# Kernel tuning notes

Measured on AMD Instinct MI355X. Metric: run time of the kernel, lower is better.

Reference implementation:

```python
import jax, jax.numpy as jnp
import numpy as np

H, C = 4, 32            # heads, per-head out channels -> H*C = 128
NEG = jnp.float32(-1e9) # stand-in for -inf mask (keeps grads finite)
NUM_LOC = 15            # self.num_locations hardcoded to 15


def _tconv(x, src, dst, ea, Wq, bq, Wk, bk, Wv, bv, We, Ws, bs, Wb):
    # PyG TransformerConv(beta=True, concat=True, edge_dim=1)
    N = x.shape[0]
    q = (x @ Wq + bq).reshape(N, H, C)
    k = (x @ Wk + bk).reshape(N, H, C)
    v = (x @ Wv + bv).reshape(N, H, C)
    e = (ea @ We).reshape(-1, H, C)  # edge embedding [E,H,C]
    kj = k[src] + e
    alpha = jnp.einsum('ehc,ehc->eh', q[dst], kj) / jnp.sqrt(jnp.float32(C))
    # scatter-softmax over incoming edges of each dst node
    amax = jax.ops.segment_max(alpha, dst, num_segments=N)
    ex = jnp.exp(alpha - amax[dst])
    den = jax.ops.segment_sum(ex, dst, num_segments=N)
    w = ex / (den[dst] + 1e-16)
    out = jax.ops.segment_sum((v[src] + e) * w[..., None], dst, num_segments=N).reshape(N, H * C)
    xr = x @ Ws + bs  # lin_skip
    beta = jax.nn.sigmoid(jnp.concatenate([out, xr, out - xr], axis=-1) @ Wb)  # [N,1]
    return beta * xr + (1.0 - beta) * out


def _bn(x, g, b):
    # BatchNorm1d in training mode (batch statistics, biased var)
    m = x.mean(0)
    v = ((x - m) ** 2).mean(0)
    return (x - m) * jax.lax.rsqrt(v + 1e-5) * g + b


def _forward_core(fa, edge_index, active_mask):
    (node_type, requests, latency,
     c0_Wq, c0_bq, c0_Wk, c0_bk, c0_Wv, c0_bv, c0_We, c0_Ws, c0_bs, c0_Wb,
     t0_W, t0_b, bn0_g, bn0_b,
     cs_Wq, cs_bq, cs_Wk, cs_bk, cs_Wv, cs_bv, cs_We, cs_Ws, cs_bs, cs_Wb,
     ts_W, ts_b, bns_g, bns_b,
     emb_W1, emb_b1, emb_W2, emb_b2, emb_W3, emb_b3,
     rem_W, rem_b, add_W, add_b) = fa
    src, dst = edge_index[0], edge_index[1]
    ea = latency[:, None]                      # edge_attr [E,1]
    x = jnp.stack([node_type, requests], axis=1)  # [N,2]
    # NetworkGraphEmbeddingConstructor: conv1 + 4 stacked conv/linear/bn blocks
    x = _tconv(x, src, dst, ea, c0_Wq, c0_bq, c0_Wk, c0_bk, c0_Wv, c0_bv, c0_We, c0_Ws, c0_bs, c0_Wb)
    x = _bn(jax.nn.relu(x @ t0_W + t0_b), bn0_g, bn0_b)
    for i in range(4):
        x = _tconv(x, src, dst, ea, cs_Wq[i], cs_bq[i], cs_Wk[i], cs_bk[i], cs_Wv[i], cs_bv[i], cs_We[i], cs_Ws[i], cs_bs[i], cs_Wb[i])
        x = _bn(jax.nn.relu(x @ ts_W[i] + ts_b[i]), bns_g[i], bns_b[i])
    # embedding_transformation MLP
    x = jax.nn.relu(x @ emb_W1 + emb_b1)
    x = jax.nn.relu(x @ emb_W2 + emb_b2)
    x = x @ emb_W3 + emb_b3                    # [N,64]
    # sampling head (batch_index=None branch)
    N = x.shape[0]
    maskf = jnp.where(active_mask == 1, jnp.float32(0.0), NEG)
    loc = jnp.arange(N) < NUM_LOC
    remove_mask = jnp.where(loc, jnp.where(maskf == 0.0, NEG, jnp.float32(0.0)), maskf)
    logits1 = (x @ rem_W + rem_b)[:, 0] + remove_mask
    k1, k2 = jax.random.split(jax.random.key(42))
    a1 = jnp.argmax(logits1 + jax.random.gumbel(k1, (N,), logits1.dtype))  # Categorical sample
    mask2 = maskf.at[a1].set(0.0)
    t = jnp.tanh(x[a1] @ add_W + add_b)        # [64]
    logits2 = x @ t + mask2
    a2 = jnp.argmax(logits2 + jax.random.gumbel(k2, (N,), logits2.dtype))
    log_probs = jnp.stack([jax.nn.log_softmax(logits1)[a1], jax.nn.log_softmax(logits2)[a2]])
    return jnp.stack([logits1, logits2]), jnp.stack([a1, a2]), log_probs


def setup_inputs() -> dict:
    N, E = 50000, 400000
    F, HC, EMB, L = 2, 128, 32, 4
    key = jax.random.key(0)
    kit = iter(jax.random.split(key, 64))
    def w(shape, s=0.1):
        return jax.random.normal(next(kit), shape, jnp.float32) * s
    return {
        'node_type': w((N,), 1.0),
        'requests': jax.random.uniform(next(kit), (N,), jnp.float32),
        'latency': jax.random.uniform(next(kit), (E,), jnp.float32),
        'edge_index': jax.random.randint(next(kit), (2, E), 0, N, jnp.int32),
        'active_mask': jax.random.randint(next(kit), (N,), 0, 2, jnp.int32),
        'c0_Wq': w((F, HC)), 'c0_bq': w((HC,)),
        'c0_Wk': w((F, HC)), 'c0_bk': w((HC,)),
        'c0_Wv': w((F, HC)), 'c0_bv': w((HC,)),
        'c0_We': w((1, HC)),
        'c0_Ws': w((F, HC)), 'c0_bs': w((HC,)),
        'c0_Wb': w((3 * HC, 1)),
        't0_W': w((HC, EMB)), 't0_b': w((EMB,)),
        'bn0_g': jnp.ones((EMB,), jnp.float32), 'bn0_b': jnp.zeros((EMB,), jnp.float32),
        'cs_Wq': w((L, EMB, HC)), 'cs_bq': w((L, HC)),
        'cs_Wk': w((L, EMB, HC)), 'cs_bk': w((L, HC)),
        'cs_Wv': w((L, EMB, HC)), 'cs_bv': w((L, HC)),
        'cs_We': w((L, 1, HC)),
        'cs_Ws': w((L, EMB, HC)), 'cs_bs': w((L, HC)),
        'cs_Wb': w((L, 3 * HC, 1)),
        'ts_W': w((L, HC, EMB)), 'ts_b': w((L, EMB)),
        'bns_g': jnp.ones((L, EMB), jnp.float32), 'bns_b': jnp.zeros((L, EMB), jnp.float32),
        'emb_W1': w((EMB, 128)), 'emb_b1': w((128,)),
        'emb_W2': w((128, 64)), 'emb_b2': w((64,)),
        'emb_W3': w((64, 64)), 'emb_b3': w((64,)),
        'rem_W': w((64, 1)), 'rem_b': w((1,)),
        'add_W': w((64, 64)), 'add_b': w((64,)),
    }


def reference(node_type, requests, latency, edge_index, active_mask,
              c0_Wq, c0_bq, c0_Wk, c0_bk, c0_Wv, c0_bv, c0_We, c0_Ws, c0_bs, c0_Wb,
              t0_W, t0_b, bn0_g, bn0_b,
              cs_Wq, cs_bq, cs_Wk, cs_bk, cs_Wv, cs_bv, cs_We, cs_Ws, cs_bs, cs_Wb,
              ts_W, ts_b, bns_g, bns_b,
              emb_W1, emb_b1, emb_W2, emb_b2, emb_W3, emb_b3,
              rem_W, rem_b, add_W, add_b):
    fa = (node_type, requests, latency,
          c0_Wq, c0_bq, c0_Wk, c0_bk, c0_Wv, c0_bv, c0_We, c0_Ws, c0_bs, c0_Wb,
          t0_W, t0_b, bn0_g, bn0_b,
          cs_Wq, cs_bq, cs_Wk, cs_bk, cs_Wv, cs_bv, cs_We, cs_Ws, cs_bs, cs_Wb,
          ts_W, ts_b, bns_g, bns_b,
          emb_W1, emb_b1, emb_W2, emb_b2, emb_W3, emb_b3,
          rem_W, rem_b, add_W, add_b)
    return _forward_core(fa, edge_index, active_mask)
```

## Files before the change

kernel.cpp:

```cpp
#include <hip/hip_runtime.h>
#include <hip/hip_fp16.h>
#include <cstdint>
#include <math.h>

typedef _Float16 h2 __attribute__((ext_vector_type(2)));
typedef float f32x2 __attribute__((ext_vector_type(2)));

__device__ __forceinline__ h2 f2h2(float a, float b) {
    h2 r; r.x = (_Float16)a; r.y = (_Float16)b; return r;
}
__device__ __forceinline__ float fdot2f(h2 a, h2 b, float c) {
    return __builtin_amdgcn_fdot2(a, b, c, false);
}
__device__ __forceinline__ f32x2 bc2(float x) { f32x2 r; r.x = x; r.y = x; return r; }
__device__ __forceinline__ f32x2 cvt2(h2 v) {
    f32x2 r; r.x = (float)v.x; r.y = (float)v.y; return r;
}
__device__ __forceinline__ f32x2 mk2(float a, float b) { f32x2 r; r.x = a; r.y = b; return r; }

union f4h {
    float4 f;
    h2 h[4];
    __half2 u[4];
};

__device__ __forceinline__ uint32_t rotl32(uint32_t x, uint32_t n) {
    return (x << n) | (x >> (32u - n));
}

__device__ __forceinline__ void tf2x32(uint32_t k0, uint32_t k1,
                                       uint32_t x0, uint32_t x1,
                                       uint32_t& o0, uint32_t& o1) {
    uint32_t k2 = k0 ^ k1 ^ 0x1BD11BDAu;
    x0 += k0; x1 += k1;
    x0 += x1; x1 = rotl32(x1, 13); x1 ^= x0;
    x0 += x1; x1 = rotl32(x1, 15); x1 ^= x0;
    x0 += x1; x1 = rotl32(x1, 26); x1 ^= x0;
    x0 += x1; x1 = rotl32(x1, 6);  x1 ^= x0;
    x0 += k1; x1 += k2 + 1u;
    x0 += x1; x1 = rotl32(x1, 17); x1 ^= x0;
    x0 += x1; x1 = rotl32(x1, 29); x1 ^= x0;
    x0 += x1; x1 = rotl32(x1, 16); x1 ^= x0;
    x0 += x1; x1 = rotl32(x1, 24); x1 ^= x0;
    x0 += k2; x1 += k0 + 2u;
    x0 += x1; x1 = rotl32(x1, 13); x1 ^= x0;
    x0 += x1; x1 = rotl32(x1, 15); x1 ^= x0;
    x0 += x1; x1 = rotl32(x1, 26); x1 ^= x0;
    x0 += x1; x1 = rotl32(x1, 6);  x1 ^= x0;
    x0 += k0; x1 += k1 + 3u;
    x0 += x1; x1 = rotl32(x1, 17); x1 ^= x0;
    x0 += x1; x1 = rotl32(x1, 29); x1 ^= x0;
    x0 += x1; x1 = rotl32(x1, 16); x1 ^= x0;
    x0 += x1; x1 = rotl32(x1, 24); x1 ^= x0;
    x0 += k1; x1 += k2 + 4u;
    x0 += x1; x1 = rotl32(x1, 13); x1 ^= x0;
    x0 += x1; x1 = rotl32(x1, 15); x1 ^= x0;
    x0 += x1; x1 = rotl32(x1, 26); x1 ^= x0;
    x0 += x1; x1 = rotl32(x1, 6);  x1 ^= x0;
    x0 += k2; x1 += k0 + 5u;
    o0 = x0; o1 = x1;
}

__device__ float gumbel_at(int n, int which, int N) {
    uint32_t a0, a1, b0, b1;
    tf2x32(0u, 42u, 0u, 2u, a0, a1);
    tf2x32(0u, 42u, 1u, 3u, b0, b1);
    uint32_t gk0 = which ? a1 : a0;
    uint32_t gk1 = which ? b1 : b0;
    int half = N >> 1;
    uint32_t o0, o1, bits;
    if (n < half) { tf2x32(gk0, gk1, (uint32_t)n, (uint32_t)(n + half), o0, o1); bits = o0; }
    else          { tf2x32(gk0, gk1, (uint32_t)(n - half), (uint32_t)n, o0, o1); bits = o1; }
    float f = __uint_as_float((bits >> 9) | 0x3F800000u) - 1.0f;
    float u = fmaxf(1.17549435e-38f, f);
    return -logf(-logf(u));
}

__device__ __forceinline__ uint32_t fmono(float f) {
    uint32_t b = __float_as_uint(f);
    return (b & 0x80000000u) ? ~b : (b | 0x80000000u);
}
__device__ __forceinline__ float funmono(uint32_t u) {
    uint32_t b = (u & 0x80000000u) ? (u & 0x7FFFFFFFu) : ~u;
    return __uint_as_float(b);
}

#define NEGF (-1e9f)
#define ATTNGRID 2048

__global__ void k_hist(const int* __restrict__ dstp, int* __restrict__ deg, int E) {
    int e = blockIdx.x * 256 + threadIdx.x;
    if (e < E) atomicAdd(&deg[dstp[e]], 1);
}

__global__ void k_scan1(const int* __restrict__ deg, int* __restrict__ bsum, int N) {
    __shared__ int s[256];
    int i = blockIdx.x * 256 + threadIdx.x;
    s[threadIdx.x] = (i < N) ? deg[i] : 0;
    __syncthreads();
    for (int st = 128; st > 0; st >>= 1) {
        if (threadIdx.x < st) s[threadIdx.x] += s[threadIdx.x + st];
        __syncthreads();
    }
    if (threadIdx.x == 0) bsum[blockIdx.x] = s[0];
}

__global__ void k_scan2(int* __restrict__ bsum, int nb) {
    __shared__ int s[256];
    int i = threadIdx.x;
    int v = (i < nb) ? bsum[i] : 0;
    s[i] = v;
    __syncthreads();
    for (int st = 1; st < 256; st <<= 1) {
        int t = (i >= st) ? s[i - st] : 0;
        __syncthreads();
        s[i] += t;
        __syncthreads();
    }
    if (i < nb) bsum[i] = s[i] - v;
}

__global__ void k_scan3(const int* __restrict__ deg, const int* __restrict__ bsum,
                        int* __restrict__ rowptr, int* __restrict__ cursor, int N) {
    __shared__ int s[256];
    int i = blockIdx.x * 256 + threadIdx.x;
    int v = (i < N) ? deg[i] : 0;
    s[threadIdx.x] = v;
    __syncthreads();
    for (int st = 1; st < 256; st <<= 1) {
        int t = (threadIdx.x >= st) ? s[threadIdx.x - st] : 0;
        __syncthreads();
        s[threadIdx.x] += t;
        __syncthreads();
    }
    int excl = s[threadIdx.x] - v + bsum[blockIdx.x];
    if (i < N) { rowptr[i] = excl; cursor[i] = excl; }
}

__global__ void k_fill(const int* __restrict__ dstp, const int* __restrict__ srcp,
                       const float* __restrict__ lat, int* __restrict__ cursor,
                       int2* __restrict__ srclat, int E) {
    int e = blockIdx.x * 256 + threadIdx.x;
    if (e < E) {
        int pos = atomicAdd(&cursor[dstp[e]], 1);
        srclat[pos] = make_int2(srcp[e], __float_as_int(lat[e]));
    }
}

__global__ __launch_bounds__(512, 4) void k_qkvr(
        const float* __restrict__ xin, const float* __restrict__ nt,
        const float* __restrict__ rq, int din, int N,
        const float* __restrict__ Wq, const float* __restrict__ bq,
        const float* __restrict__ Wk, const float* __restrict__ bk,
        const float* __restrict__ Wv, const float* __restrict__ bv,
        const float* __restrict__ Ws, const float* __restrict__ bs,
        const double* __restrict__ SUM, const double* __restrict__ SUMSQ,
        const float* __restrict__ bng, const float* __restrict__ bnb,
        int applyBN,
        __half* __restrict__ Q, __half* __restrict__ KV, __half* __restrict__ R) {
    __shared__ h2 w2[4][16 * 128];
    __shared__ float bias[4][128];
    __shared__ h2 xs2[32][17];
    __shared__ float sscale[32], sshift[32];
    int t = threadIdx.x;
    int dpCount = din >> 1;
    for (int i = t; i < dpCount * 128; i += 512) {
        int dp = i >> 7, j = i & 127;
        w2[0][i] = f2h2(Wq[(size_t)(2 * dp) * 128 + j], Wq[(size_t)(2 * dp + 1) * 128 + j]);
        w2[1][i] = f2h2(Wk[(size_t)(2 * dp) * 128 + j], Wk[(size_t)(2 * dp + 1) * 128 + j]);
        w2[2][i] = f2h2(Wv[(size_t)(2 * dp) * 128 + j], Wv[(size_t)(2 * dp + 1) * 128 + j]);
        w2[3][i] = f2h2(Ws[(size_t)(2 * dp) * 128 + j], Ws[(size_t)(2 * dp + 1) * 128 + j]);
    }
    if (t < 128) {
        bias[0][t] = bq[t]; bias[1][t] = bk[t]; bias[2][t] = bv[t]; bias[3][t] = bs[t];
    }
    if (t < 32) {
        if (applyBN) {
            double m = SUM[t] / N;
            double v = SUMSQ[t] / N - m * m;
            float inv = rsqrtf((float)v + 1e-5f);
            float sc = inv * bng[t];
            sscale[t] = sc;
            sshift[t] = bnb[t] - (float)m * sc;
        } else {
            sscale[t] = 1.f; sshift[t] = 0.f;
        }
    }
    int quad = t & 31;
    int sub = t >> 5;
    int dpsh = (din == 32) ? 4 : 0;
    int tiles = (N + 31) >> 5;
    for (int tile = blockIdx.x; tile < tiles; tile += gridDim.x) {
        int base = tile << 5;
        __syncthreads();
        for (int i = t; i < 32 * dpCount; i += 512) {
            int nl = i >> dpsh, dp = i & (dpCount - 1);
            int nn = base + nl;
            float x0 = 0.f, x1 = 0.f;
            if (nn < N) {
                if (din == 2) { x0 = nt[nn]; x1 = rq[nn]; }
                else {
                    x0 = xin[(size_t)nn * din + 2 * dp];
                    x1 = xin[(size_t)nn * din + 2 * dp + 1];
                }
            }
            x0 = x0 * sscale[2 * dp] + sshift[2 * dp];
            x1 = x1 * sscale[2 * dp + 1] + sshift[2 * dp + 1];
            xs2[nl][dp] = f2h2(x0, x1);
        }
        __syncthreads();
        float acc[4][2][4];
#pragma unroll
        for (int m = 0; m < 4; ++m)
#pragma unroll
            for (int k = 0; k < 2; ++k)
#pragma unroll
                for (int c = 0; c < 4; ++c) acc[m][k][c] = bias[m][quad * 4 + c];
        for (int dp = 0; dp < dpCount; ++dp) {
            h2 xv0 = xs2[sub * 2 + 0][dp];
            h2 xv1 = xs2[sub * 2 + 1][dp];
#pragma unroll
            for (int m = 0; m < 4; ++m) {
                const h2* wp = &w2[m][dp * 128 + quad * 4];
                h2 wa = wp[0], wb = wp[1], wc = wp[2], wd = wp[3];
                acc[m][0][0] = fdot2f(xv0, wa, acc[m][0][0]);
                acc[m][0][1] = fdot2f(xv0, wb, acc[m][0][1]);
                acc[m][0][2] = fdot2f(xv0, wc, acc[m][0][2]);
                acc[m][0][3] = fdot2f(xv0, wd, acc[m][0][3]);
                acc[m][1][0] = fdot2f(xv1, wa, acc[m][1][0]);
                acc[m][1][1] = fdot2f(xv1, wb, acc[m][1][1]);
                acc[m][1][2] = fdot2f(xv1, wc, acc[m][1][2]);
                acc[m][1][3] = fdot2f(xv1, wd, acc[m][1][3]);
            }
        }
#pragma unroll
        for (int k = 0; k < 2; ++k) {
            int n = base + sub * 2 + k;
            if (n < N) {
                *(__half2*)&Q[(size_t)n * 128 + quad * 4 + 0] =
// ... 164 lines not shown
        float inv = 1.f / (den + 1e-16f);
        f32x2 inv2 = bc2(inv), pls2 = bc2(plsum);
        f32x2 O0 = (A0 + pls2 * wep[0]) * inv2;
        f32x2 O1 = (A1 + pls2 * wep[1]) * inv2;
        f32x2 O2 = (A2 + pls2 * wep[2]) * inv2;
        f32x2 O3 = (A3 + pls2 * wep[3]) * inv2;

        f32x2 R0 = cvt2(rh.h[0]), R1 = cvt2(rh.h[1]);
        f32x2 R2 = cvt2(rh.h[2]), R3 = cvt2(rh.h[3]);
        f32x2 G = O0 * bop[0];
        G += R0 * brp[0];
        G += O1 * bop[1]; G += R1 * brp[1];
        G += O2 * bop[2]; G += R2 * brp[2];
        G += O3 * bop[3]; G += R3 * brp[3];
        float g = G.x + G.y;
        g += __shfl_xor(g, 1); g += __shfl_xor(g, 2);
        g += __shfl_xor(g, 4); g += __shfl_xor(g, 8);
        float beta = 1.0f / (1.0f + __expf(-g));

        if ((l64 & 16) == 0 && n < N) {
            f32x2 bb = bc2(beta), ib = bc2(1.0f - beta);
            f32x2 W0 = bb * R0 + ib * O0;
            f32x2 W1 = bb * R1 + ib * O1;
            f32x2 W2 = bb * R2 + ib * O2;
            f32x2 W3 = bb * R3 + ib * O3;
            *(__half2*)&A[(size_t)n * 128 + lane * 8 + 0] = __floats2half2_rn(W0.x, W0.y);
            *(__half2*)&A[(size_t)n * 128 + lane * 8 + 2] = __floats2half2_rn(W1.x, W1.y);
            *(__half2*)&A[(size_t)n * 128 + lane * 8 + 4] = __floats2half2_rn(W2.x, W2.y);
            *(__half2*)&A[(size_t)n * 128 + lane * 8 + 6] = __floats2half2_rn(W3.x, W3.y);
        }

        qh.f = pq.f; rh.f = pr.f; k0.f = pk.f; v0.f = pv.f; l0 = pl;
        start = s1; d = d1;
        s1 = s2; d1 = d2; s2 = s3; d2 = d3;
        psl1 = psl2;
    }
}

__global__ __launch_bounds__(256) void k_linstats(
        const __half* __restrict__ A, const float* __restrict__ tW,
        const float* __restrict__ tb, float* __restrict__ H32,
        double* __restrict__ partials, int N) {
    __shared__ h2 w2l[64 * 32];
    __shared__ float bias[32];
    __shared__ h2 xsT[64][66];
    __shared__ double sp1[4][8][4], sp2[4][8][4];
    int t = threadIdx.x;
    for (int i = t; i < 64 * 32; i += 256) {
        int dp = i >> 5, j = i & 31;
        w2l[i] = f2h2(tW[(size_t)(2 * dp) * 32 + j], tW[(size_t)(2 * dp + 1) * 32 + j]);
    }
    if (t < 32) bias[t] = tb[t];
    int quad = t & 7;
    int sub = t >> 3;
    int base = blockIdx.x << 6;

    __syncthreads();
#pragma unroll
    for (int k = 0; k < 4; ++k) {
        int i = t + 256 * k;
        int nl = i >> 4, g8 = i & 15;
        int n = base + nl;
        h2 hv[4];
        if (n < N) {
            const h2* ap = (const h2*)(A + (size_t)n * 128 + g8 * 8);
            hv[0] = ap[0]; hv[1] = ap[1]; hv[2] = ap[2]; hv[3] = ap[3];
        } else {
            h2 z; z.x = (_Float16)0.f; z.y = (_Float16)0.f;
            hv[0] = z; hv[1] = z; hv[2] = z; hv[3] = z;
        }
        xsT[g8 * 4 + 0][nl] = hv[0];
        xsT[g8 * 4 + 1][nl] = hv[1];
        xsT[g8 * 4 + 2][nl] = hv[2];
        xsT[g8 * 4 + 3][nl] = hv[3];
    }
    __syncthreads();

    float acc[2][4];
#pragma unroll
    for (int k = 0; k < 2; ++k)
#pragma unroll
        for (int c = 0; c < 4; ++c) acc[k][c] = bias[quad * 4 + c];
    for (int dp = 0; dp < 64; ++dp) {
        h2 x0 = xsT[dp][sub * 2 + 0];
        h2 x1 = xsT[dp][sub * 2 + 1];
        const h2* wp = &w2l[dp * 32 + quad * 4];
        h2 wa = wp[0], wb = wp[1], wc = wp[2], wd = wp[3];
        acc[0][0] = fdot2f(x0, wa, acc[0][0]);
        acc[0][1] = fdot2f(x0, wb, acc[0][1]);
        acc[0][2] = fdot2f(x0, wc, acc[0][2]);
        acc[0][3] = fdot2f(x0, wd, acc[0][3]);
        acc[1][0] = fdot2f(x1, wa, acc[1][0]);
        acc[1][1] = fdot2f(x1, wb, acc[1][1]);
        acc[1][2] = fdot2f(x1, wc, acc[1][2]);
        acc[1][3] = fdot2f(x1, wd, acc[1][3]);
    }
    double s1[4] = {0, 0, 0, 0}, s2[4] = {0, 0, 0, 0};
#pragma unroll
    for (int k = 0; k < 2; ++k) {
        int n = base + sub * 2 + k;
        if (n < N) {
            float4 yv;
            yv.x = fmaxf(acc[k][0], 0.f); yv.y = fmaxf(acc[k][1], 0.f);
            yv.z = fmaxf(acc[k][2], 0.f); yv.w = fmaxf(acc[k][3], 0.f);
            *(float4*)&H32[(size_t)n * 32 + quad * 4] = yv;
            s1[0] += yv.x; s1[1] += yv.y; s1[2] += yv.z; s1[3] += yv.w;
            s2[0] += (double)yv.x * yv.x; s2[1] += (double)yv.y * yv.y;
            s2[2] += (double)yv.z * yv.z; s2[3] += (double)yv.w * yv.w;
        }
    }
#pragma unroll
    for (int c = 0; c < 4; ++c) {
        s1[c] += __shfl_xor(s1[c], 8);  s2[c] += __shfl_xor(s2[c], 8);
        s1[c] += __shfl_xor(s1[c], 16); s2[c] += __shfl_xor(s2[c], 16);
        s1[c] += __shfl_xor(s1[c], 32); s2[c] += __shfl_xor(s2[c], 32);
    }
    __syncthreads();
    int wave = t >> 6;
    if ((t & 63) < 8) {
#pragma unroll
        for (int c = 0; c < 4; ++c) { sp1[wave][quad][c] = s1[c]; sp2[wave][quad][c] = s2[c]; }
    }
    __syncthreads();
    if (t < 32) {
        int q = t >> 2, c = t & 3;
        double a1 = 0, a2 = 0;
#pragma unroll
        for (int wv = 0; wv < 4; ++wv) { a1 += sp1[wv][q][c]; a2 += sp2[wv][q][c]; }
        partials[(size_t)blockIdx.x * 64 + t] = a1;
        partials[(size_t)blockIdx.x * 64 + 32 + t] = a2;
    }
}

__global__ void k_statred(const double* __restrict__ partials,
                          double* __restrict__ SUM, double* __restrict__ SUMSQ,
                          int nblocks) {
    __shared__ double s[256];
    int col = blockIdx.x;
    double a = 0;
    for (int b = threadIdx.x; b < nblocks; b += 256)
        a += partials[(size_t)b * 64 + col];
    s[threadIdx.x] = a;
    __syncthreads();
    for (int st = 128; st > 0; st >>= 1) {
        if (threadIdx.x < st) s[threadIdx.x] += s[threadIdx.x + st];
        __syncthreads();
    }
    if (threadIdx.x == 0) {
        if (col < 32) SUM[col] = s[0];
        else SUMSQ[col - 32] = s[0];
    }
}

__global__ __launch_bounds__(256) void k_mlp1(
        const float* __restrict__ H32,
        const double* __restrict__ SUM, const double* __restrict__ SUMSQ,
        const float* __restrict__ bng, const float* __restrict__ bnb,
        const float* __restrict__ W1, const float* __restrict__ b1,
        float* __restrict__ Y1, unsigned int* __restrict__ smallbuf, int N) {
    __shared__ float w1[32 * 128];
    __shared__ float sb1[128];
    __shared__ float sscale[32], sshift[32];
    __shared__ float xs[32][36];
    int t = threadIdx.x;
    if (blockIdx.x == 0 && t < 16) smallbuf[t] = 0u;
    for (int i = t; i < 32 * 128; i += 256) w1[i] = W1[i];
    if (t < 128) sb1[t] = b1[t];
    if (t < 32) {
        double m = SUM[t] / N;
        double v = SUMSQ[t] / N - m * m;
        float inv = rsqrtf((float)v + 1e-5f);
        float sc = inv * bng[t];
        sscale[t] = sc;
        sshift[t] = bnb[t] - (float)m * sc;
    }
    int quad = t & 31, sub = t >> 5;
    int tiles = (N + 31) >> 5;
    for (int tile = blockIdx.x; tile < tiles; tile += gridDim.x) {
        int base = tile << 5;
        __syncthreads();
        {
            int nl = t >> 3, q = t & 7;
            int n = base + nl;
            float4 xv = make_float4(0.f, 0.f, 0.f, 0.f);
            if (n < N) xv = *(const float4*)&H32[(size_t)n * 32 + q * 4];
            xs[nl][q * 4 + 0] = xv.x * sscale[q * 4 + 0] + sshift[q * 4 + 0];
            xs[nl][q * 4 + 1] = xv.y * sscale[q * 4 + 1] + sshift[q * 4 + 1];
            xs[nl][q * 4 + 2] = xv.z * sscale[q * 4 + 2] + sshift[q * 4 + 2];
            xs[nl][q * 4 + 3] = xv.w * sscale[q * 4 + 3] + sshift[q * 4 + 3];
        }
        __syncthreads();
        float a[4][4];
#pragma unroll
        for (int k = 0; k < 4; ++k)
#pragma unroll
            for (int c = 0; c < 4; ++c) a[k][c] = sb1[quad * 4 + c];
        for (int d = 0; d < 32; ++d) {
            float4 w4 = *(const float4*)&w1[d * 128 + quad * 4];
#pragma unroll
            for (int k = 0; k < 4; ++k) {
                float x = xs[sub * 4 + k][d];
                a[k][0] = fmaf(x, w4.x, a[k][0]);
                a[k][1] = fmaf(x, w4.y, a[k][1]);
                a[k][2] = fmaf(x, w4.z, a[k][2]);
                a[k][3] = fmaf(x, w4.w, a[k][3]);
            }
        }
#pragma unroll
        for (int k = 0; k < 4; ++k) {
            int n = base + sub * 4 + k;
            if (n < N) {
                float4 yv;
                yv.x = fmaxf(a[k][0], 0.f); yv.y = fmaxf(a[k][1], 0.f);
                yv.z = fmaxf(a[k][2], 0.f); yv.w = fmaxf(a[k][3], 0.f);
                *(float4*)&Y1[(size_t)n * 128 + quad * 4] = yv;
            }
        }
    }
}

__global__ __launch_bounds__(256) void k_mlp2(
        const float* __restrict__ Y1, const float* __restrict__ W2,
        const float* __restrict__ b2, float* __restrict__ Y2, int N) {
    __shared__ float w2f[128 * 64];
    __shared__ float sb2[64];
    __shared__ float xs[32][132];
    int t = threadIdx.x;
    for (int i = t; i < 128 * 64; i += 256) w2f[i] = W2[i];
    if (t < 64) sb2[t] = b2[t];
    int quad = t & 15, sub = t >> 4;
    int tiles = (N + 31) >> 5;
    for (int tile = blockIdx.x; tile < tiles; tile += gridDim.x) {
        int base = tile << 5;
        __syncthreads();
#pragma unroll
        for (int k = 0; k < 4; ++k) {
            int i = t + 256 * k;
            int nl = i >> 5, q = i & 31;
            int n = base + nl;
            float4 xv = make_float4(0.f, 0.f, 0.f, 0.f);
            if (n < N) xv = *(const float4*)&Y1[(size_t)n * 128 + q * 4];
            *(float4*)&xs[nl][q * 4] = xv;
        }
        __syncthreads();
        float a[2][4];
#pragma unroll
        for (int k = 0; k < 2; ++k)
#pragma unroll
            for (int c = 0; c < 4; ++c) a[k][c] = sb2[quad * 4 + c];
        for (int d = 0; d < 128; ++d) {
            float4 w4 = *(const float4*)&w2f[d * 64 + quad * 4];
#pragma unroll
            for (int k = 0; k < 2; ++k) {
                float x = xs[sub * 2 + k][d];
                a[k][0] = fmaf(x, w4.x, a[k][0]);
                a[k][1] = fmaf(x, w4.y, a[k][1]);
                a[k][2] = fmaf(x, w4.z, a[k][2]);
                a[k][3] = fmaf(x, w4.w, a[k][3]);
            }
        }
#pragma unroll
        for (int k = 0; k < 2; ++k) {
            int n = base + sub * 2 + k;
            if (n < N) {
                float4 yv;
                yv.x = fmaxf(a[k][0], 0.f); yv.y = fmaxf(a[k][1], 0.f);
                yv.z = fmaxf(a[k][2], 0.f); yv.w = fmaxf(a[k][3], 0.f);
                *(float4*)&Y2[(size_t)n * 64 + quad * 4] = yv;
            }
        }
    }
}

__global__ __launch_bounds__(256) void k_mlp3(
        const float* __restrict__ Y2, const float* __restrict__ W3,
        const float* __restrict__ b3, float* __restrict__ X3, int N) {
    __shared__ float w3[64 * 64];
    __shared__ float sb3[64];
    __shared__ float xs[32][68];
    int t = threadIdx.x;
    for (int i = t; i < 64 * 64; i += 256) w3[i] = W3[i];
    if (t < 64) sb3[t] = b3[t];
    int quad = t & 15, sub = t >> 4;
    int tiles = (N + 31) >> 5;
    for (int tile = blockIdx.x; tile < tiles; tile += gridDim.x) {
        int base = tile << 5;
        __syncthreads();
#pragma unroll
        for (int k = 0; k < 2; ++k) {
            int i = t + 256 * k;
            int nl = i >> 4, q = i & 15;
            int n = base + nl;
            float4 xv = make_float4(0.f, 0.f, 0.f, 0.f);
            if (n < N) xv = *(const float4*)&Y2[(size_t)n * 64 + q * 4];
            *(float4*)&xs[nl][q * 4] = xv;
        }
        __syncthreads();
        float a[2][4];
#pragma unroll
        for (int k = 0; k < 2; ++k)
#pragma unroll
            for (int c = 0; c < 4; ++c) a[k][c] = sb3[quad * 4 + c];
        for (int d = 0; d < 64; ++d) {
            float4 w4 = *(const float4*)&w3[d * 64 + quad * 4];
#pragma unroll
            for (int k = 0; k < 2; ++k) {
                float x = xs[sub * 2 + k][d];
                a[k][0] = fmaf(x, w4.x, a[k][0]);
                a[k][1] = fmaf(x, w4.y, a[k][1]);
                a[k][2] = fmaf(x, w4.z, a[k][2]);
                a[k][3] = fmaf(x, w4.w, a[k][3]);
            }
        }
#pragma unroll
        for (int k = 0; k < 2; ++k) {
            int n = base + sub * 2 + k;
            if (n < N)
                *(float4*)&X3[(size_t)n * 64 + quad * 4] = *(float4*)a[k];
        }
    }
}

__global__ void k_head1(const float* __restrict__ X3, const float* __restrict__ remW,
                        const float* __restrict__ remB, const int* __restrict__ active,
                        float* __restrict__ l1out, unsigned long long* __restrict__ slot1,
                        unsigned int* __restrict__ m1, int N) {
    int n = blockIdx.x * 256 + threadIdx.x;
    if (n >= N) return;
    const float* xr = X3 + (size_t)n * 64;
    float acc = remB[0];
    for (int d = 0; d < 64; d++) acc = fmaf(xr[d], remW[d], acc);
    float maskf = (active[n] == 1) ? 0.f : NEGF;
    float rm = (n < 15) ? ((maskf == 0.f) ? NEGF : 0.f) : maskf;
    float l1 = acc + rm;
    l1out[n] = l1;
    atomicMax(m1, fmono(l1));
    float z = l1 + gumbel_at(n, 0, N);
    unsigned long long p = ((unsigned long long)fmono(z) << 32) |
                           (unsigned long long)(0xFFFFFFFFu - (unsigned)n);
    atomicMax(slot1, p);
}

__global__ void k_head2(const float* __restrict__ X3, const float* __restrict__ addW,
                        const float* __restrict__ addB,
                        const unsigned long long* __restrict__ slot1,
                        float* __restrict__ tvec, int* __restrict__ a1buf) {
    int j = threadIdx.x;
    unsigned long long p = *slot1;
    int a1 = (int)(0xFFFFFFFFu - (unsigned)(p & 0xFFFFFFFFull));
    const float* xr = X3 + (size_t)a1 * 64;
    float acc = addB[j];
    for (int d = 0; d < 64; d++) acc = fmaf(xr[d], addW[d * 64 + j], acc);
    tvec[j] = tanhf(acc);
    if (j == 0) *a1buf = a1;
}

__global__ void k_head3(const float* __restrict__ X3, const float* __restrict__ tvec,
                        const int* __restrict__ active, const int* __restrict__ a1buf,
                        float* __restrict__ l2out, unsigned long long* __restrict__ slot2,
                        unsigned int* __restrict__ m2, int N) {
    int n = blockIdx.x * 256 + threadIdx.x;
    if (n >= N) return;
    const float* xr = X3 + (size_t)n * 64;
    float acc = 0.f;
    for (int d = 0; d < 64; d++) acc = fmaf(xr[d], tvec[d], acc);
    float maskf = (active[n] == 1) ? 0.f : NEGF;
    if (n == *a1buf) maskf = 0.f;
    float l2 = acc + maskf;
    l2out[n] = l2;
    atomicMax(m2, fmono(l2));
    float z = l2 + gumbel_at(n, 1, N);
    unsigned long long p = ((unsigned long long)fmono(z) << 32) |
                           (unsigned long long)(0xFFFFFFFFu - (unsigned)n);
    atomicMax(slot2, p);
}

__global__ void k_sumexp(const float* __restrict__ l1, const float* __restrict__ l2,
                         const unsigned int* __restrict__ m1, const unsigned int* __restrict__ m2,
                         float* __restrict__ se, int N) {
    int t = blockIdx.x * 256 + threadIdx.x;
    float M1 = funmono(*m1), M2 = funmono(*m2);
    float e1 = 0.f, e2 = 0.f;
    if (t < N) { e1 = expf(l1[t] - M1); e2 = expf(l2[t] - M2); }
    __shared__ float r1[256], r2[256];
    r1[threadIdx.x] = e1; r2[threadIdx.x] = e2;
    __syncthreads();
    for (int s = 128; s > 0; s >>= 1) {
        if (threadIdx.x < s) { r1[threadIdx.x] += r1[threadIdx.x + s]; r2[threadIdx.x] += r2[threadIdx.x + s]; }
        __syncthreads();
    }
    if (threadIdx.x == 0) { atomicAdd(&se[0], r1[0]); atomicAdd(&se[1], r2[0]); }
}

__global__ void k_final(const float* __restrict__ l1, const float* __restrict__ l2,
                        const unsigned long long* __restrict__ slot2,
                        const int* __restrict__ a1buf,
                        const unsigned int* __restrict__ m1, const unsigned int* __restrict__ m2,
                        const float* __restrict__ se, float* __restrict__ outTail, int N) {
    int a1 = *a1buf;
    int a2 = (int)(0xFFFFFFFFu - (unsigned)((*slot2) & 0xFFFFFFFFull));
    outTail[0] = (float)a1;
    outTail[1] = (float)a2;
    outTail[2] = l1[a1] - (funmono(*m1) + logf(se[0]));
    outTail[3] = l2[a2] - (funmono(*m2) + logf(se[1]));
}

extern "C" void kernel_launch(void* const* d_in, const int* in_sizes, int n_in,
                              void* d_out, int out_size, void* d_ws, size_t ws_size,
                              hipStream_t stream) {
    const float* node_type = (const float*)d_in[0];
    const float* requests  = (const float*)d_in[1];
    const float* latency   = (const float*)d_in[2];
    const int* edge_index  = (const int*)d_in[3];
    const int* active      = (const int*)d_in[4];
    int N = in_sizes[0];
    int E = in_sizes[2];
    const int* src = edge_index;
    const int* dst = edge_index + E;
    float* out = (float*)d_out;

    char* base = (char*)d_ws;
    size_t off = 0;
    auto alloc = [&](size_t bytes) -> char* {
        char* p = base + off;
        off += (bytes + 255) & ~(size_t)255;
        return p;
    };
    char* Abuf   = alloc((size_t)N * 128 * 4);
    char* Qbuf   = alloc((size_t)N * 128 * 4);
    __half* KV   = (__half*)alloc((size_t)N * 256 * 2);
    char* Rbuf   = alloc((size_t)N * 128 * 4);
    float* H32   = (float*)alloc((size_t)N * 32 * 4);
    int* deg     = (int*)alloc((size_t)N * 4);
    int* rowptr  = (int*)alloc((size_t)N * 4);
    int* cursor  = (int*)alloc((size_t)N * 4);
    int2* srclat = (int2*)alloc((size_t)E * 8);
    int* bsum    = (int*)alloc(1024 * 4);
    int lsTiles = (N + 63) / 64;
    double* partials = (double*)alloc((size_t)lsTiles * 64 * 8);
    double* SUM  = (double*)alloc(512);
    double* SUMSQ = SUM + 32;
    char* small  = alloc(1024);
    unsigned long long* slot1 = (unsigned long long*)small;
    unsigned long long* slot2 = slot1 + 1;
    unsigned int* m1 = (unsigned int*)(small + 16);
    unsigned int* m2 = m1 + 1;
    float* se = (float*)(small + 24);
    int* a1buf = (int*)(small + 32);
    float* tvec = (float*)(small + 64);

    __half* Ah = (__half*)Abuf;   float* Y2f = (float*)Abuf;
    __half* Qh = (__half*)Qbuf;   float* Y1f = (float*)Qbuf;
    __half* Rh = (__half*)Rbuf;   float* X3f = (float*)Rbuf;

    int ng = (N + 255) / 256;
    int egE = (E + 255) / 256;
    int nb = ng;

    (void)hipMemsetAsync(deg, 0, (size_t)N * 4, stream);
    k_hist<<<egE, 256, 0, stream>>>(dst, deg, E);
    k_scan1<<<nb, 256, 0, stream>>>(deg, bsum, N);
    k_scan2<<<1, 256, 0, stream>>>(bsum, nb);
    k_scan3<<<nb, 256, 0, stream>>>(deg, bsum, rowptr, cursor, N);
    k_fill<<<egE, 256, 0, stream>>>(dst, src, latency, cursor, srclat, E);

    for (int L = 0; L < 5; ++L) {
        int din = L ? 32 : 2;
        const float* xin = L ? H32 : nullptr;
        const float* Wq = L ? (const float*)d_in[19] + (size_t)(L - 1) * 4096 : (const float*)d_in[5];
        const float* bq = L ? (const float*)d_in[20] + (size_t)(L - 1) * 128  : (const float*)d_in[6];
        const float* Wk = L ? (const float*)d_in[21] + (size_t)(L - 1) * 4096 : (const float*)d_in[7];
        const float* bk = L ? (const float*)d_in[22] + (size_t)(L - 1) * 128  : (const float*)d_in[8];
        const float* Wv = L ? (const float*)d_in[23] + (size_t)(L - 1) * 4096 : (const float*)d_in[9];
        const float* bv = L ? (const float*)d_in[24] + (size_t)(L - 1) * 128  : (const float*)d_in[10];
        const float* We = L ? (const float*)d_in[25] + (size_t)(L - 1) * 128  : (const float*)d_in[11];
        const float* Ws = L ? (const float*)d_in[26] + (size_t)(L - 1) * 4096 : (const float*)d_in[12];
        const float* bs = L ? (const float*)d_in[27] + (size_t)(L - 1) * 128  : (const float*)d_in[13];
        const float* Wb = L ? (const float*)d_in[28] + (size_t)(L - 1) * 384  : (const float*)d_in[14];
        const float* tW = L ? (const float*)d_in[29] + (size_t)(L - 1) * 4096 : (const float*)d_in[15];
        const float* tb = L ? (const float*)d_in[30] + (size_t)(L - 1) * 32   : (const float*)d_in[16];
        const float* bngP = (L == 1) ? (const float*)d_in[17]
                          : (L >= 2) ? (const float*)d_in[31] + (size_t)(L - 2) * 32 : nullptr;
        const float* bnbP = (L == 1) ? (const float*)d_in[18]
                          : (L >= 2) ? (const float*)d_in[32] + (size_t)(L - 2) * 32 : nullptr;

        k_qkvr<<<1024, 512, 0, stream>>>(xin, node_type, requests, din, N,
                                         Wq, bq, Wk, bk, Wv, bv, Ws, bs,
                                         SUM, SUMSQ, bngP, bnbP, (L > 0) ? 1 : 0,
                                         Qh, KV, Rh);
        k_attn<<<ATTNGRID, 256, 0, stream>>>(srclat, Qh, KV, We, Rh, Wb,
                                             rowptr, deg, Ah, N);
        k_linstats<<<lsTiles, 256, 0, stream>>>(Ah, tW, tb, H32, partials, N);
        k_statred<<<64, 256, 0, stream>>>(partials, SUM, SUMSQ, lsTiles);
    }

    k_mlp1<<<512, 256, 0, stream>>>(H32, SUM, SUMSQ,
                                    (const float*)d_in[31] + 3 * 32,
                                    (const float*)d_in[32] + 3 * 32,
                                    (const float*)d_in[33], (const float*)d_in[34],
                                    Y1f, (unsigned int*)small, N);
    k_mlp2<<<512, 256, 0, stream>>>(Y1f, (const float*)d_in[35], (const float*)d_in[36],
                                    Y2f, N);
    k_mlp3<<<512, 256, 0, stream>>>(Y2f, (const float*)d_in[37], (const float*)d_in[38],
                                    X3f, N);
    k_head1<<<ng, 256, 0, stream>>>(X3f, (const float*)d_in[39], (const float*)d_in[40],
                                    active, out, slot1, m1, N);
    k_head2<<<1, 64, 0, stream>>>(X3f, (const float*)d_in[41], (const float*)d_in[42],
                                  slot1, tvec, a1buf);
    k_head3<<<ng, 256, 0, stream>>>(X3f, tvec, active, a1buf, out + N, slot2, m2, N);
    k_sumexp<<<ng, 256, 0, stream>>>(out, out + N, m1, m2, se, N);
    k_final<<<1, 1, 0, stream>>>(out, out + N, slot2, a1buf, m1, m2, se, out + 2 * N, N);
}
```

Measured before the change: 713.5 us.

## Fuse MLP layers and head kernels with online log-sum-exp partial reductions

Fuses MLP layers 1 and 2 into one kernel that keeps the 128-wide hidden activations in shared memory, and folds the removal-head logit computation into the layer-3 kernel. The global-atomic max plus separate sum-exp pass is replaced by per-block online log-sum-exp partials merged in a final block-wide kernel. This removes the Y1 global round trip, several launches and contended atomics, but the fused kernel uses more shared memory, which may lower occupancy, and it now processes 16-node tiles.

```diff
diff --git a/kernel.cpp b/kernel.cpp
--- a/kernel.cpp
+++ b/kernel.cpp
@@ -85,6 +85,13 @@
     return __uint_as_float(b);
 }
 
+__device__ __forceinline__ void lse_merge(float& m, float& s, float m2, float s2) {
+    float M = fmaxf(m, m2);
+    float a = (m == -INFINITY) ? 0.f : expf(m - M) * s;
+    float b = (m2 == -INFINITY) ? 0.f : expf(m2 - M) * s2;
+    m = M; s = a + b;
+}
+
 #define NEGF (-1e9f)
 #define ATTNGRID 2048
 
@@ -555,20 +562,26 @@
     }
 }
 
-__global__ __launch_bounds__(256) void k_mlp1(
+__global__ __launch_bounds__(256) void k_mlp12(
         const float* __restrict__ H32,
         const double* __restrict__ SUM, const double* __restrict__ SUMSQ,
         const float* __restrict__ bng, const float* __restrict__ bnb,
         const float* __restrict__ W1, const float* __restrict__ b1,
-        float* __restrict__ Y1, unsigned int* __restrict__ smallbuf, int N) {
+        const float* __restrict__ W2, const float* __restrict__ b2,
+        float* __restrict__ Y2, unsigned int* __restrict__ smallbuf, int N) {
     __shared__ float w1[32 * 128];
     __shared__ float sb1[128];
     __shared__ float sscale[32], sshift[32];
-    __shared__ float xs[32][36];
+    __shared__ float w2f[128 * 64];
+    __shared__ float sb2[64];
+    __shared__ float xs[16][36];
+    __shared__ float y1[16][132];
     int t = threadIdx.x;
     if (blockIdx.x == 0 && t < 16) smallbuf[t] = 0u;
     for (int i = t; i < 32 * 128; i += 256) w1[i] = W1[i];
+    for (int i = t; i < 128 * 64; i += 256) w2f[i] = W2[i];
     if (t < 128) sb1[t] = b1[t];
+    if (t < 64) sb2[t] = b2[t];
     if (t < 32) {
         double m = SUM[t] / N;
         double v = SUMSQ[t] / N - m * m;
@@ -577,12 +590,13 @@
         sscale[t] = sc;
         sshift[t] = bnb[t] - (float)m * sc;
     }
-    int quad = t & 31, sub = t >> 5;
-    int tiles = (N + 31) >> 5;
+    int q1 = t & 31, s1_ = t >> 5;
+    int q2 = t & 15, s2_ = t >> 4;
+    int tiles = (N + 15) >> 4;
     for (int tile = blockIdx.x; tile < tiles; tile += gridDim.x) {
-        int base = tile << 5;
-        __syncthreads();
-        {
+        int base = tile << 4;
+        __syncthreads();
+        if (t < 128) {
             int nl = t >> 3, q = t & 7;
             int n = base + nl;
             float4 xv = make_float4(0.f, 0.f, 0.f, 0.f);
@@ -593,16 +607,16 @@
             xs[nl][q * 4 + 3] = xv.w * sscale[q * 4 + 3] + sshift[q * 4 + 3];
         }
         __syncthreads();
-        float a[4][4];
-#pragma unroll
-        for (int k = 0; k < 4; ++k)
-#pragma unroll
-            for (int c = 0; c < 4; ++c) a[k][c] = sb1[quad * 4 + c];
+        float a[2][4];
+#pragma unroll
+        for (int k = 0; k < 2; ++k)
+#pragma unroll
+            for (int c = 0; c < 4; ++c) a[k][c] = sb1[q1 * 4 + c];
         for (int d = 0; d < 32; ++d) {
-            float4 w4 = *(const float4*)&w1[d * 128 + quad * 4];
-#pragma unroll
-            for (int k = 0; k < 4; ++k) {
-                float x = xs[sub * 4 + k][d];
+            float4 w4 = *(const float4*)&w1[d * 128 + q1 * 4];
+#pragma unroll
+            for (int k = 0; k < 2; ++k) {
+                float x = xs[s1_ * 2 + k][d];
                 a[k][0] = fmaf(x, w4.x, a[k][0]);
                 a[k][1] = fmaf(x, w4.y, a[k][1]);
                 a[k][2] = fmaf(x, w4.z, a[k][2]);
@@ -610,39 +624,66 @@
             }
         }
 #pragma unroll
-        for (int k = 0; k < 4; ++k) {
-            int n = base + sub * 4 + k;
-            if (n < N) {
-                float4 yv;
-                yv.x = fmaxf(a[k][0], 0.f); yv.y = fmaxf(a[k][1], 0.f);
-                yv.z = fmaxf(a[k][2], 0.f); yv.w = fmaxf(a[k][3], 0.f);
-                *(float4*)&Y1[(size_t)n * 128 + quad * 4] = yv;
-            }
-        }
-    }
-}
-
-__global__ __launch_bounds__(256) void k_mlp2(
-        const float* __restrict__ Y1, const float* __restrict__ W2,
-        const float* __restrict__ b2, float* __restrict__ Y2, int N) {
-    __shared__ float w2f[128 * 64];
-    __shared__ float sb2[64];
-    __shared__ float xs[32][132];
+        for (int k = 0; k < 2; ++k) {
+            float4 yv;
+            yv.x = fmaxf(a[k][0], 0.f); yv.y = fmaxf(a[k][1], 0.f);
+            yv.z = fmaxf(a[k][2], 0.f); yv.w = fmaxf(a[k][3], 0.f);
+            *(float4*)&y1[s1_ * 2 + k][q1 * 4] = yv;
+        }
+        __syncthreads();
+        float b[4];
+#pragma unroll
+        for (int c = 0; c < 4; ++c) b[c] = sb2[q2 * 4 + c];
+        for (int d = 0; d < 128; ++d) {
+            float4 w4 = *(const float4*)&w2f[d * 64 + q2 * 4];
+            float x = y1[s2_][d];
+            b[0] = fmaf(x, w4.x, b[0]);
+            b[1] = fmaf(x, w4.y, b[1]);
+            b[2] = fmaf(x, w4.z, b[2]);
+            b[3] = fmaf(x, w4.w, b[3]);
+        }
+        int n = base + s2_;
+        if (n < N) {
+            float4 yv;
+            yv.x = fmaxf(b[0], 0.f); yv.y = fmaxf(b[1], 0.f);
+            yv.z = fmaxf(b[2], 0.f); yv.w = fmaxf(b[3], 0.f);
+            *(float4*)&Y2[(size_t)n * 64 + q2 * 4] = yv;
+        }
+    }
+}
+
+__global__ __launch_bounds__(256) void k_mlp3h(
+        const float* __restrict__ Y2, const float* __restrict__ W3,
+        const float* __restrict__ b3,
+        const float* __restrict__ remW, const float* __restrict__ remB,
+        const int* __restrict__ active,
+        float* __restrict__ X3, float* __restrict__ l1out,
+        unsigned long long* __restrict__ slot1, float2* __restrict__ part1,
+        int N) {
+    __shared__ float w3[64 * 64];
+    __shared__ float sb3[64];
+    __shared__ float xs[32][68];
+    __shared__ float srw[64];
+    __shared__ float redm[256], reds[256];
+    __shared__ unsigned long long redb[256];
     int t = threadIdx.x;
-    for (int i = t; i < 128 * 64; i += 256) w2f[i] = W2[i];
-    if (t < 64) sb2[t] = b2[t];
+    for (int i = t; i < 64 * 64; i += 256) w3[i] = W3[i];
+    if (t < 64) { sb3[t] = b3[t]; srw[t] = remW[t]; }
+    float rB = remB[0];
     int quad = t & 15, sub = t >> 4;
+    float lm = -INFINITY, ls = 0.f;
+    unsigned long long best = 0ull;
     int tiles = (N + 31) >> 5;
     for (int tile = blockIdx.x; tile < tiles; tile += gridDim.x) {
         int base = tile << 5;
         __syncthreads();
 #pragma unroll
-        for (int k = 0; k < 4; ++k) {
+        for (int k = 0; k < 2; ++k) {
             int i = t + 256 * k;
-            int nl = i >> 5, q = i & 31;
+            int nl = i >> 4, q = i & 15;
             int n = base + nl;
             float4 xv = make_float4(0.f, 0.f, 0.f, 0.f);
-            if (n < N) xv = *(const float4*)&Y1[(size_t)n * 128 + q * 4];
+            if (n < N) xv = *(const float4*)&Y2[(size_t)n * 64 + q * 4];
             *(float4*)&xs[nl][q * 4] = xv;
         }
         __syncthreads();
@@ -650,9 +691,9 @@
 #pragma unroll
         for (int k = 0; k < 2; ++k)
 #pragma unroll
-            for (int c = 0; c < 4; ++c) a[k][c] = sb2[quad * 4 + c];
-        for (int d = 0; d < 128; ++d) {
-            float4 w4 = *(const float4*)&w2f[d * 64 + quad * 4];
+            for (int c = 0; c < 4; ++c) a[k][c] = sb3[quad * 4 + c];
+        for (int d = 0; d < 64; ++d) {
+            float4 w4 = *(const float4*)&w3[d * 64 + quad * 4];
 #pragma unroll
             for (int k = 0; k < 2; ++k) {
                 float x = xs[sub * 2 + k][d];
@@ -665,83 +706,45 @@
 #pragma unroll
         for (int k = 0; k < 2; ++k) {
             int n = base + sub * 2 + k;
-            if (n < N) {
-                float4 yv;
-                yv.x = fmaxf(a[k][0], 0.f); yv.y = fmaxf(a[k][1], 0.f);
-                yv.z = fmaxf(a[k][2], 0.f); yv.w = fmaxf(a[k][3], 0.f);
-                *(float4*)&Y2[(size_t)n * 64 + quad * 4] = yv;
-            }
-        }
-    }
-}
-
-__global__ __launch_bounds__(256) void k_mlp3(
-        const float* __restrict__ Y2, const float* __restrict__ W3,
-        const float* __restrict__ b3, float* __restrict__ X3, int N) {
-    __shared__ float w3[64 * 64];
-    __shared__ float sb3[64];
-    __shared__ float xs[32][68];
-    int t = threadIdx.x;
-    for (int i = t; i < 64 * 64; i += 256) w3[i] = W3[i];
-    if (t < 64) sb3[t] = b3[t];
-    int quad = t & 15, sub = t >> 4;
-    int tiles = (N + 31) >> 5;
-    for (int tile = blockIdx.x; tile < tiles; tile += gridDim.x) {
-        int base = tile << 5;
-        __syncthreads();
-#pragma unroll
-        for (int k = 0; k < 2; ++k) {
-            int i = t + 256 * k;
-            int nl = i >> 4, q = i & 15;
-            int n = base + nl;
-            float4 xv = make_float4(0.f, 0.f, 0.f, 0.f);
-            if (n < N) xv = *(const float4*)&Y2[(size_t)n * 64 + q * 4];
-            *(float4*)&xs[nl][q * 4] = xv;
-        }
-        __syncthreads();
-        float a[2][4];
-#pragma unroll
-        for (int k = 0; k < 2; ++k)
-#pragma unroll
-            for (int c = 0; c < 4; ++c) a[k][c] = sb3[quad * 4 + c];
-        for (int d = 0; d < 64; ++d) {
-            float4 w4 = *(const float4*)&w3[d * 64 + quad * 4];
-#pragma unroll
-            for (int k = 0; k < 2; ++k) {
-                float x = xs[sub * 2 + k][d];
-                a[k][0] = fmaf(x, w4.x, a[k][0]);
-                a[k][1] = fmaf(x, w4.y, a[k][1]);
-                a[k][2] = fmaf(x, w4.z, a[k][2]);
-                a[k][3] = fmaf(x, w4.w, a[k][3]);
-            }
+            if (n < N)
+                *(float4*)&X3[(size_t)n * 64 + quad * 4] = *(float4*)a[k];
         }
 #pragma unroll
         for (int k = 0; k < 2; ++k) {
             int n = base + sub * 2 + k;
-            if (n < N)
-                *(float4*)&X3[(size_t)n * 64 + quad * 4] = *(float4*)a[k];
-        }
-    }
-}
-
-__global__ void k_head1(const float* __restrict__ X3, const float* __restrict__ remW,
-                        const float* __restrict__ remB, const int* __restrict__ active,
-                        float* __restrict__ l1out, unsigned long long* __restrict__ slot1,
-                        unsigned int* __restrict__ m1, int N) {
-    int n = blockIdx.x * 256 + threadIdx.x;
-    if (n >= N) return;
-    const float* xr = X3 + (size_t)n * 64;
-    float acc = remB[0];
-    for (int d = 0; d < 64; d++) acc = fmaf(xr[d], remW[d], acc);
-    float maskf = (active[n] == 1) ? 0.f : NEGF;
-    float rm = (n < 15) ? ((maskf == 0.f) ? NEGF : 0.f) : maskf;
-    float l1 = acc + rm;
-    l1out[n] = l1;
-    atomicMax(m1, fmono(l1));
-    float z = l1 + gumbel_at(n, 0, N);
-    unsigned long long p = ((unsigned long long)fmono(z) << 32) |
-                           (unsigned long long)(0xFFFFFFFFu - (unsigned)n);
-    atomicMax(slot1, p);
+            float h = a[k][0] * srw[quad * 4 + 0] + a[k][1] * srw[quad * 4 + 1]
+                    + a[k][2] * srw[quad * 4 + 2] + a[k][3] * srw[quad * 4 + 3];
+            h += __shfl_xor(h, 1); h += __shfl_xor(h, 2);
+            h += __shfl_xor(h, 4); h += __shfl_xor(h, 8);
+            if (quad == 0 && n < N) {
+                float maskf = (active[n] == 1) ? 0.f : NEGF;
+                float rm_ = (n < 15) ? ((maskf == 0.f) ? NEGF : 0.f) : maskf;
+                float l1 = h + rB + rm_;
+                l1out[n] = l1;
+                lse_merge(lm, ls, l1, 1.0f);
+                float z = l1 + gumbel_at(n, 0, N);
+                unsigned long long p = ((unsigned long long)fmono(z) << 32) |
+                                       (unsigned long long)(0xFFFFFFFFu - (unsigned)n);
+                if (p > best) best = p;
+            }
+        }
+    }
+    redm[t] = lm; reds[t] = ls; redb[t] = best;
+    __syncthreads();
+    for (int st = 128; st > 0; st >>= 1) {
+        if (t < st) {
+            float m2 = redm[t + st], s2 = reds[t + st];
+            float mm = redm[t], ss = reds[t];
+            lse_merge(mm, ss, m2, s2);
+            redm[t] = mm; reds[t] = ss;
+            if (redb[t + st] > redb[t]) redb[t] = redb[t + st];
+        }
+        __syncthreads();
+    }
+    if (t == 0) {
+        part1[blockIdx.x] = make_float2(redm[0], reds[0]);
+        if (redb[0]) atomicMax(slot1, redb[0]);
+    }
 }
 
 __global__ void k_head2(const float* __restrict__ X3, const float* __restrict__ addW,
@@ -758,54 +761,81 @@
     if (j == 0) *a1buf = a1;
 }
 
-__global__ void k_head3(const float* __restrict__ X3, const float* __restrict__ tvec,
-                        const int* __restrict__ active, const int* __restrict__ a1buf,
-                        float* __restrict__ l2out, unsigned long long* __restrict__ slot2,
-                        unsigned int* __restrict__ m2, int N) {
-    int n = blockIdx.x * 256 + threadIdx.x;
-    if (n >= N) return;
-    const float* xr = X3 + (size_t)n * 64;
-    float acc = 0.f;
-    for (int d = 0; d < 64; d++) acc = fmaf(xr[d], tvec[d], acc);
-    float maskf = (active[n] == 1) ? 0.f : NEGF;
-    if (n == *a1buf) maskf = 0.f;
-    float l2 = acc + maskf;
-    l2out[n] = l2;
-    atomicMax(m2, fmono(l2));
-    float z = l2 + gumbel_at(n, 1, N);
-    unsigned long long p = ((unsigned long long)fmono(z) << 32) |
-                           (unsigned long long)(0xFFFFFFFFu - (unsigned)n);
-    atomicMax(slot2, p);
-}
-
-__global__ void k_sumexp(const float* __restrict__ l1, const float* __restrict__ l2,
-                         const unsigned int* __restrict__ m1, const unsigned int* __restrict__ m2,
-                         float* __restrict__ se, int N) {
-    int t = blockIdx.x * 256 + threadIdx.x;
-    float M1 = funmono(*m1), M2 = funmono(*m2);
-    float e1 = 0.f, e2 = 0.f;
-    if (t < N) { e1 = expf(l1[t] - M1); e2 = expf(l2[t] - M2); }
-    __shared__ float r1[256], r2[256];
-    r1[threadIdx.x] = e1; r2[threadIdx.x] = e2;
-    __syncthreads();
-    for (int s = 128; s > 0; s >>= 1) {
-        if (threadIdx.x < s) { r1[threadIdx.x] += r1[threadIdx.x + s]; r2[threadIdx.x] += r2[threadIdx.x + s]; }
-        __syncthreads();
-    }
-    if (threadIdx.x == 0) { atomicAdd(&se[0], r1[0]); atomicAdd(&se[1], r2[0]); }
-}
-
-__global__ void k_final(const float* __restrict__ l1, const float* __restrict__ l2,
-                        const unsigned long long* __restrict__ slot2,
-                        const int* __restrict__ a1buf,
-                        const unsigned int* __restrict__ m1, const unsigned int* __restrict__ m2,
-                        const float* __restrict__ se, float* __restrict__ outTail, int N) {
-    int a1 = *a1buf;
-    int a2 = (int)(0xFFFFFFFFu - (unsigned)((*slot2) & 0xFFFFFFFFull));
-    outTail[0] = (float)a1;
-    outTail[1] = (float)a2;
-    outTail[2] = l1[a1] - (funmono(*m1) + logf(se[0]));
-    outTail[3] = l2[a2] - (funmono(*m2) + logf(se[1]));
+__global__ void k_head3p(const float* __restrict__ X3, const float* __restrict__ tvec,
+                         const int* __restrict__ active, const int* __restrict__ a1buf,
+                         float* __restrict__ l2out, unsigned long long* __restrict__ slot2,
+                         float2* __restrict__ part2, int N) {
+    __shared__ float redm[256], reds[256];
+    __shared__ unsigned long long redb[256];
+    int t = threadIdx.x;
+    int n = blockIdx.x * 256 + t;
+    float lm = -INFINITY, ls = 0.f;
+    unsigned long long best = 0ull;
+    if (n < N) {
+        const float* xr = X3 + (size_t)n * 64;
+        float acc = 0.f;
+        for (int d = 0; d < 64; d++) acc = fmaf(xr[d], tvec[d], acc);
+        float maskf = (active[n] == 1) ? 0.f : NEGF;
+        if (n == *a1buf) maskf = 0.f;
+        float l2 = acc + maskf;
+        l2out[n] = l2;
+        lm = l2; ls = 1.f;
+        float z = l2 + gumbel_at(n, 1, N);
+        best = ((unsigned long long)fmono(z) << 32) |
+               (unsigned long long)(0xFFFFFFFFu - (unsigned)n);
+    }
+    redm[t] = lm; reds[t] = ls; redb[t] = best;
+    __syncthreads();
+    for (int st = 128; st > 0; st >>= 1) {
+        if (t < st) {
+            float mm = redm[t], ss = reds[t];
+            lse_merge(mm, ss, redm[t + st], reds[t + st]);
+            redm[t] = mm; reds[t] = ss;
+            if (redb[t + st] > redb[t]) redb[t] = redb[t + st];
+        }
+        __syncthreads();
+    }
+    if (t == 0) {
+        part2[blockIdx.x] = make_float2(redm[0], reds[0]);
+        if (redb[0]) atomicMax(slot2, redb[0]);
+    }
+}
+
+__global__ void k_final2(const float* __restrict__ l1, const float* __restrict__ l2,
+                         const unsigned long long* __restrict__ slot2,
+                         const int* __restrict__ a1buf,
+                         const float2* __restrict__ part1, int np1,
+                         const float2* __restrict__ part2, int np2,
+                         float* __restrict__ outTail) {
+    __shared__ float rm[256], rs[256];
+    int t = threadIdx.x;
+    float m = -INFINITY, s = 0.f;
+    for (int i = t; i < np1; i += 256) { float2 p = part1[i]; lse_merge(m, s, p.x, p.y); }
+    rm[t] = m; rs[t] = s;
+    __syncthreads();
+    for (int st = 128; st > 0; st >>= 1) {
+        if (t < st) { float mm = rm[t], ss = rs[t]; lse_merge(mm, ss, rm[t + st], rs[t + st]); rm[t] = mm; rs[t] = ss; }
+        __syncthreads();
+    }
+    float M1 = rm[0], S1 = rs[0];
+    __syncthreads();
+    m = -INFINITY; s = 0.f;
+    for (int i = t; i < np2; i += 256) { float2 p = part2[i]; lse_merge(m, s, p.x, p.y); }
+    rm[t] = m; rs[t] = s;
+    __syncthreads();
+    for (int st = 128; st > 0; st >>= 1) {
+        if (t < st) { float mm = rm[t], ss = rs[t]; lse_merge(mm, ss, rm[t + st], rs[t + st]); rm[t] = mm; rs[t] = ss; }
+        __syncthreads();
+    }
+    float M2 = rm[0], S2 = rs[0];
+    if (t == 0) {
+        int a1 = *a1buf;
+        int a2 = (int)(0xFFFFFFFFu - (unsigned)((*slot2) & 0xFFFFFFFFull));
+        outTail[0] = (float)a1;
+        outTail[1] = (float)a2;
+        outTail[2] = l1[a1] - (M1 + logf(S1));
+        outTail[3] = l2[a2] - (M2 + logf(S2));
+    }
 }
 
 extern "C" void kernel_launch(void* const* d_in, const int* in_sizes, int n_in,
@@ -843,20 +873,19 @@
     double* partials = (double*)alloc((size_t)lsTiles * 64 * 8);
     double* SUM  = (double*)alloc(512);
     double* SUMSQ = SUM + 32;
+    float2* part1 = (float2*)alloc(512 * 8);
+    int ng = (N + 255) / 256;
+    float2* part2 = (float2*)alloc((size_t)ng * 8);
     char* small  = alloc(1024);
     unsigned long long* slot1 = (unsigned long long*)small;
     unsigned long long* slot2 = slot1 + 1;
-    unsigned int* m1 = (unsigned int*)(small + 16);
-    unsigned int* m2 = m1 + 1;
-    float* se = (float*)(small + 24);
     int* a1buf = (int*)(small + 32);
     float* tvec = (float*)(small + 64);
 
     __half* Ah = (__half*)Abuf;   float* Y2f = (float*)Abuf;
-    __half* Qh = (__half*)Qbuf;   float* Y1f = (float*)Qbuf;
+    __half* Qh = (__half*)Qbuf;
     __half* Rh = (__half*)Rbuf;   float* X3f = (float*)Rbuf;
 
-    int ng = (N + 255) / 256;
     int egE = (E + 255) / 256;
     int nb = ng;
 
@@ -897,20 +926,19 @@
         k_statred<<<64, 256, 0, stream>>>(partials, SUM, SUMSQ, lsTiles);
     }
 
-    k_mlp1<<<512, 256, 0, stream>>>(H32, SUM, SUMSQ,
-                                    (const float*)d_in[31] + 3 * 32,
-                                    (const float*)d_in[32] + 3 * 32,
-                                    (const float*)d_in[33], (const float*)d_in[34],
-                                    Y1f, (unsigned int*)small, N);
-    k_mlp2<<<512, 256, 0, stream>>>(Y1f, (const float*)d_in[35], (const float*)d_in[36],
-                                    Y2f, N);
-    k_mlp3<<<512, 256, 0, stream>>>(Y2f, (const float*)d_in[37], (const float*)d_in[38],
-                                    X3f, N);
-    k_head1<<<ng, 256, 0, stream>>>(X3f, (const float*)d_in[39], (const float*)d_in[40],
-                                    active, out, slot1, m1, N);
+    k_mlp12<<<512, 256, 0, stream>>>(H32, SUM, SUMSQ,
+                                     (const float*)d_in[31] + 3 * 32,
+                                     (const float*)d_in[32] + 3 * 32,
+                                     (const float*)d_in[33], (const float*)d_in[34],
+                                     (const float*)d_in[35], (const float*)d_in[36],
+                                     Y2f, (unsigned int*)small, N);
+    k_mlp3h<<<512, 256, 0, stream>>>(Y2f, (const float*)d_in[37], (const float*)d_in[38],
+                                     (const float*)d_in[39], (const float*)d_in[40],
+                                     active, X3f, out, slot1, part1, N);
     k_head2<<<1, 64, 0, stream>>>(X3f, (const float*)d_in[41], (const float*)d_in[42],
                                   slot1, tvec, a1buf);
-    k_head3<<<ng, 256, 0, stream>>>(X3f, tvec, active, a1buf, out + N, slot2, m2, N);
-    k_sumexp<<<ng, 256, 0, stream>>>(out, out + N, m1, m2, se, N);
-    k_final<<<1, 1, 0, stream>>>(out, out + N, slot2, a1buf, m1, m2, se, out + 2 * N, N);
-}
+    k_head3p<<<ng, 256, 0, stream>>>(X3f, tvec, active, a1buf, out + N, slot2,
+                                     part2, N);
+    k_final2<<<1, 256, 0, stream>>>(out, out + N, slot2, a1buf,
+                                    part1, 512, part2, ng, out + 2 * N);
+}
```

After: 676.9 us. 5.1% less time.
